# Optimization experiments

Measured on AMD Instinct MI355X. Metric: run time of the kernel, lower is better.

The kernel has to match this reference:

```python
import jax, jax.numpy as jnp
import numpy as np


def _lstm(x, W_ih, W_hh, b_ih, b_hh):
    """PyTorch-convention LSTM. x: [B, T, I] -> (ys [B, T, H], h_T [B, H]).
    Gate order i, f, g, o as in torch.nn.LSTM."""
    def step(carry, xt):
        h, c = carry
        gates = xt @ W_ih.T + b_ih + h @ W_hh.T + b_hh
        i, f, g, o = jnp.split(gates, 4, axis=-1)
        c = jax.nn.sigmoid(f) * c + jax.nn.sigmoid(i) * jnp.tanh(g)
        h = jax.nn.sigmoid(o) * jnp.tanh(c)
        return (h, c), h
    B = x.shape[0]
    H = W_hh.shape[1]
    init = (jnp.zeros((B, H), x.dtype), jnp.zeros((B, H), x.dtype))
    (hT, _), ys = jax.lax.scan(step, init, jnp.swapaxes(x, 0, 1))
    return jnp.swapaxes(ys, 0, 1), hT


def setup_inputs():
    key = jax.random.key(0)
    ks = jax.random.split(key, 13)
    B, S, F = 256, 1024, 16
    p = lambda k, shape: jax.random.normal(k, shape, jnp.float32) * 0.1
    return {
        "x": jax.random.normal(ks[0], (B, S, F), jnp.float32),
        "data": 0,
        "W_ih1": p(ks[1], (32, 1)),  "W_hh1": p(ks[2], (32, 8)),
        "b_ih1": p(ks[3], (32,)),    "b_hh1": p(ks[4], (32,)),
        "W_ih2": p(ks[5], (512, 8)), "W_hh2": p(ks[6], (512, 128)),
        "b_ih2": p(ks[7], (512,)),   "b_hh2": p(ks[8], (512,)),
        "W1": p(ks[9], (64, 128)),   "b1": p(ks[10], (64,)),
        "W2": p(ks[11], (1, 64)),    "b2": p(ks[12], (1,)),
    }


def reference(x, data, W_ih1, W_hh1, b_ih1, b_hh1,
              W_ih2, W_hh2, b_ih2, b_hh2, W1, b1, W2, b2):
    B, S, F = x.shape
    # rnn1: original loops over batch; here all B*S rows are one big batch of
    # length-F sequences with feature dim 1. We only need the final hidden h_T.
    x1 = x.reshape(B * S, F, 1)
    _, h1 = _lstm(x1, W_ih1, W_hh1, b_ih1, b_hh1)            # [B*S, 8]
    # original does .detach().numpy() -> gradient is cut here
    h1 = jax.lax.stop_gradient(h1).reshape(B, S, 8)
    ys2, _ = _lstm(h1, W_ih2, W_hh2, b_ih2, b_hh2)           # [B, S, 128]
    last = ys2[:, -1, :]                                     # [B, 128]
    return (last @ W1.T + b1) @ W2.T + b2                    # [B, 1]
```

## Files before the change

### kernel.cpp

```cpp
#include <hip/hip_runtime.h>
#include <cstdint>

typedef _Float16 f16x2 __attribute__((ext_vector_type(2)));

__device__ __forceinline__ float fsig(float x) {
  return __fdividef(1.f, 1.f + __expf(-x));
}
__device__ __forceinline__ float ftanh_(float x) {
  return fmaf(2.f, fsig(x + x), -1.f);
}
__device__ __forceinline__ int packf16(float a, float b) {
  f16x2 p; p.x = (_Float16)a; p.y = (_Float16)b;
  return __builtin_bit_cast(int, p);
}
__device__ __forceinline__ float dot2(int w, int h, float acc) {
  return __builtin_amdgcn_fdot2(__builtin_bit_cast(f16x2, w),
                                __builtin_bit_cast(f16x2, h), acc, false);
}
template <int CTRL>
__device__ __forceinline__ float qp(float v) {
  return __int_as_float(__builtin_amdgcn_update_dpp(
      0, __float_as_int(v), CTRL, 0xF, 0xF, true));
}
#define QP_X1 0xB1
#define QP_X2 0x4E

__global__ __launch_bounds__(256, 2) void lstm1_kernel(
    const float* __restrict__ x, const float* __restrict__ Wih,
    const float* __restrict__ Whh, const float* __restrict__ bih,
    const float* __restrict__ bhh, int4* __restrict__ h1out) {
  const int n = blockIdx.x * 256 + threadIdx.x;

  int whh2[128];
#pragma unroll
  for (int r = 0; r < 32; ++r) {
#pragma unroll
    for (int j = 0; j < 4; ++j) {
      float2 v = ((const float2*)(Whh + r * 8))[j];
      whh2[r * 4 + j] = packf16(v.x, v.y);
    }
  }
  int wxb[32];
#pragma unroll
  for (int r = 0; r < 32; ++r) wxb[r] = packf16(Wih[r], bih[r] + bhh[r]);

#pragma unroll
  for (int i = 0; i < 128; i += 8)
    asm volatile("" : "+v"(whh2[i]), "+v"(whh2[i + 1]), "+v"(whh2[i + 2]),
                      "+v"(whh2[i + 3]), "+v"(whh2[i + 4]), "+v"(whh2[i + 5]),
                      "+v"(whh2[i + 6]), "+v"(whh2[i + 7]));
#pragma unroll
  for (int i = 0; i < 32; i += 8)
    asm volatile("" : "+v"(wxb[i]), "+v"(wxb[i + 1]), "+v"(wxb[i + 2]),
                      "+v"(wxb[i + 3]), "+v"(wxb[i + 4]), "+v"(wxb[i + 5]),
                      "+v"(wxb[i + 6]), "+v"(wxb[i + 7]));

  const float* __restrict__ xp = x + (size_t)n * 16;
  float c[8];
  int h2[4];
#pragma unroll
  for (int k = 0; k < 8; ++k) c[k] = 0.f;
#pragma unroll
  for (int j = 0; j < 4; ++j) h2[j] = 0;

  float xv = xp[0];
#pragma unroll 1
  for (int t = 0; t < 16; ++t) {
    float xn = xp[(t + 1) & 15];
    const int xt1 = packf16(xv, 1.f);
    float hn[8];
#pragma unroll
    for (int k = 0; k < 8; ++k) {
      float acc[4];
#pragma unroll
      for (int gi = 0; gi < 4; ++gi) {
        const int r = gi * 8 + k;
        float a = dot2(wxb[r], xt1, 0.f);
        a = dot2(whh2[r * 4 + 0], h2[0], a);
        a = dot2(whh2[r * 4 + 1], h2[1], a);
        a = dot2(whh2[r * 4 + 2], h2[2], a);
        a = dot2(whh2[r * 4 + 3], h2[3], a);
        acc[gi] = a;
      }
      float iv = fsig(acc[0]), fv = fsig(acc[1]);
      float gv = ftanh_(acc[2]), ov = fsig(acc[3]);
      c[k] = fmaf(fv, c[k], iv * gv);
      hn[k] = ov * ftanh_(c[k]);
    }
#pragma unroll
    for (int j = 0; j < 4; ++j) h2[j] = packf16(hn[2 * j], hn[2 * j + 1]);
    xv = xn;
  }
  int4 o;
  o.x = h2[0]; o.y = h2[1]; o.z = h2[2]; o.w = h2[3];
  h1out[n] = o;
}

__global__ __launch_bounds__(512, 2) void lstm2_kernel(
    const int4* __restrict__ h1, const float* __restrict__ Wih,
    const float* __restrict__ Whh, const float* __restrict__ bih,
    const float* __restrict__ bhh, const float* __restrict__ Wd1,
    const float* __restrict__ bd1, const float* __restrict__ Wd2,
    const float* __restrict__ bd2, float* __restrict__ out) {
  __shared__ __align__(16) _Float16 sH[2][128];
  __shared__ __align__(16) int4 sX[1024];
  const int b = blockIdx.x;
  const int t = threadIdx.x;
  const int m = t >> 2;
  const int q = t & 3;
  const int G = ((q & 1) << 1) | (q >> 1);
  const bool sel0 = (q & 1) != 0;
  const bool sel1 = (q & 2) != 0;
  const bool isq0 = (q == 0);
  const bool isq1 = (q == 1);

  {
    const int4* xq = h1 + (size_t)b * 1024;
    sX[t] = xq[t];
    sX[t + 512] = xq[t + 512];
  }

  int w[64];
#pragma unroll
  for (int g = 0; g < 4; ++g) {
    const float2* p = (const float2*)(Whh + (size_t)(g * 128 + m) * 128 + q * 32);
#pragma unroll
    for (int j = 0; j < 16; ++j) {
      float2 v = p[j];
      w[g * 16 + j] = packf16(v.x, v.y);
    }
  }

  int wig[4];
  {
    const float2* pi = (const float2*)(Wih + (size_t)(G * 128 + m) * 8);
#pragma unroll
    for (int j = 0; j < 4; ++j) {
      float2 v = pi[j];
      wig[j] = packf16(v.x, v.y);
    }
  }
  const float bias = bih[G * 128 + m] + bhh[G * 128 + m];

  int hq[16];
#pragma unroll
  for (int i = 0; i < 16; ++i) hq[i] = 0;
  float c = 0.f;

  __syncthreads();
  int4 xc = sX[0];

#pragma unroll 1
  for (int ts = 0; ts < 1024; ++ts) {
    float bx = bias;
    bx = dot2(wig[0], xc.x, bx);
    bx = dot2(wig[1], xc.y, bx);
    bx = dot2(wig[2], xc.z, bx);
    bx = dot2(wig[3], xc.w, bx);

    float R0 = 0.f, R1 = 0.f, R2 = 0.f, R3 = 0.f;
#pragma unroll
    for (int j = 0; j < 16; ++j) {
      R0 = dot2(w[j], hq[j], R0);
      R1 = dot2(w[16 + j], hq[j], R1);
      R2 = dot2(w[32 + j], hq[j], R2);
      R3 = dot2(w[48 + j], hq[j], R3);
    }
    float s0 = sel0 ? R0 : R2, s1 = sel0 ? R1 : R3;
    float k0 = sel0 ? R2 : R0, k1 = sel0 ? R3 : R1;
    float S0 = k0 + qp<QP_X1>(s0);
    float S1 = k1 + qp<QP_X1>(s1);
    float s2 = sel1 ? S0 : S1;
    float k2 = sel1 ? S1 : S0;
    float S = k2 + qp<QP_X2>(s2) + bx;

    float u = isq1 ? (S + S) : S;
    float sg = fsig(u);
    float act = isq1 ? fmaf(2.f, sg, -1.f) : sg;

    float v0 = act;
    float v1 = qp<QP_X1>(v0);
    float v2 = qp<QP_X2>(v0);
    float v3 = qp<QP_X2>(v1);
    float p01 = sel0 ? v1 : v0, p23 = sel0 ? v3 : v2;
    float q01 = sel0 ? v0 : v1, q23 = sel0 ? v2 : v3;
    float iv = sel1 ? p23 : p01;
    float fv = sel1 ? p01 : p23;
    float gv = sel1 ? q23 : q01;
    float ov = sel1 ? q01 : q23;

    c = fmaf(fv, c, iv * gv);
    float hx = ov * ftanh_(c);
    if (isq0) sH[ts & 1][m] = (_Float16)hx;
    __syncthreads();

    {
      const int4* src = (const int4*)(&sH[ts & 1][q * 32]);
      int4 A = src[0], B = src[1], C = src[2], D = src[3];
      hq[0] = A.x;  hq[1] = A.y;  hq[2] = A.z;  hq[3] = A.w;
      hq[4] = B.x;  hq[5] = B.y;  hq[6] = B.z;  hq[7] = B.w;
      hq[8] = C.x;  hq[9] = C.y;  hq[10] = C.z; hq[11] = C.w;
      hq[12] = D.x; hq[13] = D.y; hq[14] = D.z; hq[15] = D.w;
      xc = sX[ts < 1023 ? ts + 1 : 1023];
    }
  }

  if (t < 64) {
    float a = bd1[t];
#pragma unroll
    for (int k = 0; k < 128; ++k)
      a = fmaf(Wd1[t * 128 + k], (float)sH[1][k], a);
    float v = a * Wd2[t];
#pragma unroll
    for (int off = 32; off > 0; off >>= 1) v += __shfl_down(v, off);
    if (t == 0) out[b] = v + bd2[0];
  }
}

extern "C" void kernel_launch(void* const* d_in, const int* in_sizes, int n_in,
                              void* d_out, int out_size, void* d_ws, size_t ws_size,
                              hipStream_t stream) {
  const float* x    = (const float*)d_in[0];
  const float* Wih1 = (const float*)d_in[2];
  const float* Whh1 = (const float*)d_in[3];
  const float* bih1 = (const float*)d_in[4];
  const float* bhh1 = (const float*)d_in[5];
  const float* Wih2 = (const float*)d_in[6];
  const float* Whh2 = (const float*)d_in[7];
  const float* bih2 = (const float*)d_in[8];
  const float* bhh2 = (const float*)d_in[9];
  const float* W1   = (const float*)d_in[10];
  const float* b1   = (const float*)d_in[11];
  const float* W2   = (const float*)d_in[12];
  const float* b2   = (const float*)d_in[13];
  float* out = (float*)d_out;

  int4* h1 = (int4*)d_ws;

  lstm1_kernel<<<1024, 256, 0, stream>>>(x, Wih1, Whh1, bih1, bhh1, h1);
  lstm2_kernel<<<256, 512, 0, stream>>>(h1, Wih2, Whh2, bih2, bhh2,
                                        W1, b1, W2, b2, out);
}
```

Baseline: 807.1 us.

## Vectorize LSTM1 input loads and prefetch LSTM2 inputs from global

In the first LSTM, each thread's 16 scalar input loads become four float4 loads, and the loop is unrolled by four timesteps. In the second LSTM, the shared-memory staging of the per-batch h1 sequence is removed. Inputs are instead read directly from global memory with a two-step register prefetch, which frees LDS and drops the initial barrier. Launch bounds drop to one block per SM for the second kernel, and asm barriers keep the weights pinned in registers each iteration. The risk is global-load latency on the serial recurrence path if the prefetch does not hide it.

```diff
diff --git a/kernel.cpp b/kernel.cpp
--- a/kernel.cpp
+++ b/kernel.cpp
@@ -55,7 +55,7 @@
                       "+v"(wxb[i + 3]), "+v"(wxb[i + 4]), "+v"(wxb[i + 5]),
                       "+v"(wxb[i + 6]), "+v"(wxb[i + 7]));
 
-  const float* __restrict__ xp = x + (size_t)n * 16;
+  const float4* __restrict__ xp4 = (const float4*)(x + (size_t)n * 16);
   float c[8];
   int h2[4];
 #pragma unroll
@@ -63,47 +63,50 @@
 #pragma unroll
   for (int j = 0; j < 4; ++j) h2[j] = 0;
 
-  float xv = xp[0];
+  float4 xcur = xp4[0];
 #pragma unroll 1
-  for (int t = 0; t < 16; ++t) {
-    float xn = xp[(t + 1) & 15];
-    const int xt1 = packf16(xv, 1.f);
-    float hn[8];
-#pragma unroll
-    for (int k = 0; k < 8; ++k) {
-      float acc[4];
-#pragma unroll
-      for (int gi = 0; gi < 4; ++gi) {
-        const int r = gi * 8 + k;
-        float a = dot2(wxb[r], xt1, 0.f);
-        a = dot2(whh2[r * 4 + 0], h2[0], a);
-        a = dot2(whh2[r * 4 + 1], h2[1], a);
-        a = dot2(whh2[r * 4 + 2], h2[2], a);
-        a = dot2(whh2[r * 4 + 3], h2[3], a);
-        acc[gi] = a;
+  for (int tt = 0; tt < 4; ++tt) {
+    float4 xnxt = xp4[(tt + 1) & 3];
+    float xs[4] = {xcur.x, xcur.y, xcur.z, xcur.w};
+#pragma unroll
+    for (int u = 0; u < 4; ++u) {
+      const int xt1 = packf16(xs[u], 1.f);
+      float hn[8];
+#pragma unroll
+      for (int k = 0; k < 8; ++k) {
+        float acc[4];
+#pragma unroll
+        for (int gi = 0; gi < 4; ++gi) {
+          const int r = gi * 8 + k;
+          float a = dot2(wxb[r], xt1, 0.f);
+          a = dot2(whh2[r * 4 + 0], h2[0], a);
+          a = dot2(whh2[r * 4 + 1], h2[1], a);
+          a = dot2(whh2[r * 4 + 2], h2[2], a);
+          a = dot2(whh2[r * 4 + 3], h2[3], a);
+          acc[gi] = a;
+        }
+        float iv = fsig(acc[0]), fv = fsig(acc[1]);
+        float gv = ftanh_(acc[2]), ov = fsig(acc[3]);
+        c[k] = fmaf(fv, c[k], iv * gv);
+        hn[k] = ov * ftanh_(c[k]);
       }
-      float iv = fsig(acc[0]), fv = fsig(acc[1]);
-      float gv = ftanh_(acc[2]), ov = fsig(acc[3]);
-      c[k] = fmaf(fv, c[k], iv * gv);
-      hn[k] = ov * ftanh_(c[k]);
-    }
-#pragma unroll
-    for (int j = 0; j < 4; ++j) h2[j] = packf16(hn[2 * j], hn[2 * j + 1]);
-    xv = xn;
+#pragma unroll
+      for (int j = 0; j < 4; ++j) h2[j] = packf16(hn[2 * j], hn[2 * j + 1]);
+    }
+    xcur = xnxt;
   }
   int4 o;
   o.x = h2[0]; o.y = h2[1]; o.z = h2[2]; o.w = h2[3];
   h1out[n] = o;
 }
 
-__global__ __launch_bounds__(512, 2) void lstm2_kernel(
+__global__ __launch_bounds__(512, 1) void lstm2_kernel(
     const int4* __restrict__ h1, const float* __restrict__ Wih,
     const float* __restrict__ Whh, const float* __restrict__ bih,
     const float* __restrict__ bhh, const float* __restrict__ Wd1,
     const float* __restrict__ bd1, const float* __restrict__ Wd2,
     const float* __restrict__ bd2, float* __restrict__ out) {
   __shared__ __align__(16) _Float16 sH[2][128];
-  __shared__ __align__(16) int4 sX[1024];
   const int b = blockIdx.x;
   const int t = threadIdx.x;
   const int m = t >> 2;
@@ -114,12 +117,6 @@
   const bool isq0 = (q == 0);
   const bool isq1 = (q == 1);
 
-  {
-    const int4* xq = h1 + (size_t)b * 1024;
-    sX[t] = xq[t];
-    sX[t + 512] = xq[t + 512];
-  }
-
   int w[64];
 #pragma unroll
   for (int g = 0; g < 4; ++g) {
@@ -147,11 +144,19 @@
   for (int i = 0; i < 16; ++i) hq[i] = 0;
   float c = 0.f;
 
-  __syncthreads();
-  int4 xc = sX[0];
+  const int4* __restrict__ xg = h1 + (size_t)b * 1024;
+  int4 xc = xg[0];
+  int4 xn = xg[1];
 
 #pragma unroll 1
   for (int ts = 0; ts < 1024; ++ts) {
+#pragma unroll
+    for (int i = 0; i < 64; i += 8)
+      asm volatile("" : "+v"(w[i]), "+v"(w[i + 1]), "+v"(w[i + 2]),
+                        "+v"(w[i + 3]), "+v"(w[i + 4]), "+v"(w[i + 5]),
+                        "+v"(w[i + 6]), "+v"(w[i + 7]));
+    asm volatile("" : "+v"(wig[0]), "+v"(wig[1]), "+v"(wig[2]), "+v"(wig[3]));
+
     float bx = bias;
     bx = dot2(wig[0], xc.x, bx);
     bx = dot2(wig[1], xc.y, bx);
@@ -201,7 +206,8 @@
       hq[4] = B.x;  hq[5] = B.y;  hq[6] = B.z;  hq[7] = B.w;
       hq[8] = C.x;  hq[9] = C.y;  hq[10] = C.z; hq[11] = C.w;
       hq[12] = D.x; hq[13] = D.y; hq[14] = D.z; hq[15] = D.w;
-      xc = sX[ts < 1023 ? ts + 1 : 1023];
+      xc = xn;
+      xn = xg[ts < 1022 ? ts + 2 : 1023];
     }
   }
 
```

Result: no change. 817.3 us (+1.3%).
